# Kernel optimization log

Hardware: AMD Instinct MI355X
Metric: run time of the kernel (lower is better)

The kernel has to match this reference:

```python
import jax, jax.numpy as jnp
import numpy as np

B, C, T, V = 32, 96, 256, 25
BC = C // 4   # TCN branch channels
E = C // 4    # adyn embed dim (max(C//4, 8))


def hswish(x):
    return x * jnp.clip(x + 3.0, 0.0, 6.0) / 6.0


def bn(x, p):
    # p: [4, c] = (gamma, beta, running_mean, running_var); x: [B, c, T, V]
    g, b, rm, rv = p[0], p[1], p[2], p[3]
    inv = jax.lax.rsqrt(rv + 1e-5)
    return (x - rm[:, None, None]) * (g * inv)[:, None, None] + b[:, None, None]


def conv1x1(x, w):
    # w: [O, I]
    return jnp.einsum('bctv,oc->botv', x, w)


def tconv(x, w, stride, dil):
    # temporal conv, kernel 3 on T axis; w: [O, I, 3]
    return jax.lax.conv_general_dilated(
        x, w[:, :, :, None], window_strides=(stride, 1),
        padding=((dil, dil), (0, 0)), rhs_dilation=(dil, 1),
        dimension_numbers=('NCHW', 'OIHW', 'NCHW'))


def _forward(x, A_gcn, W_gcn, gcn_bn, Wp, W_adyn, adyn_gate,
             se_w1, se_b1, se_w2, se_b2,
             pa_w, pa_bn, ta_w, ta_bn, pb_w, pb_bn, tb_w, tb_bn,
             pc_w, pc_bn, pd_w, pd_bn, intra_idx, inter_idx):
    res = x
    # --- BRASP: channel-cyclic shift along joint axis (Shift-GCN style) ---
    sh = (jnp.arange(V)[None, :] + jnp.arange(C)[:, None]) % V  # [C, V]
    x = jnp.take_along_axis(x, sh[None, :, None, :], axis=3)
    # --- SGPShift: half channels gather via intra neighbors, half via inter ---
    h = C // 2
    x = jnp.concatenate([x[:, :h][..., intra_idx], x[:, h:][..., inter_idx]], axis=1)
    # --- multi-partition graph conv: y = mean_k Conv1x1_k(x @ A_k) ---
    xa = jnp.einsum('bctv,kvw->kbctw', x, A_gcn)           # [K,B,C,T,V]
    y = jnp.einsum('kbctw,koc->botw', xa, W_gcn) / A_gcn.shape[0]
    # --- dynamic adjacency (adyn) ---
    emb = jnp.einsum('bcv,ec->bev', x.mean(axis=2), Wp)    # proj then mean over T (linear)
    emb = emb / (jnp.linalg.norm(emb, axis=1, keepdims=True) + 1e-12)
    A_dyn = jnp.einsum('bev,bew->bvw', emb, emb)           # [B,V,V]
    x_dyn = jnp.einsum('bctv,bvw->bctw', x, A_dyn)
    y = y + jax.nn.sigmoid(adyn_gate) * conv1x1(x_dyn, W_adyn)
    x = hswish(bn(y, gcn_bn))
    # --- ChannelSE ---
    s = x.mean(axis=(2, 3))                                 # [B, C]
    z = jax.nn.sigmoid(jnp.dot(jax.nn.relu(jnp.dot(s, se_w1.T) + se_b1), se_w2.T) + se_b2)
    x = x * z[:, :, None, None]
    # --- MultiScaleTCN (stride 1, 4 branches of C//4 channels) ---
    a = hswish(bn(conv1x1(x, pa_w), pa_bn))
    a = bn(tconv(a, ta_w, 1, 1), ta_bn)
    b_ = hswish(bn(conv1x1(x, pb_w), pb_bn))
    b_ = bn(tconv(b_, tb_w, 1, 2), tb_bn)
    c_ = bn(conv1x1(x, pc_w), pc_bn)
    c_ = jax.lax.reduce_window(c_, -jnp.inf, jax.lax.max,
                               (1, 1, 3, 1), (1, 1, 1, 1),
                               [(0, 0), (0, 0), (1, 1), (0, 0)])
    d_ = bn(conv1x1(x, pd_w), pd_bn)
    xt = jnp.concatenate([a, b_, c_, d_], axis=1)           # [B, C, T, V]
    # --- residual + out activation (in==out, stride 1 -> identity residual) ---
    return hswish(xt + res)


def setup_inputs() -> dict:
    key = jax.random.key(0)
    ks = jax.random.split(key, 24)

    def n(k, shape, s=0.1):
        return jax.random.normal(k, shape, jnp.float32) * s

    def mkbn(k, c):
        k1, k2, k3, k4 = jax.random.split(k, 4)
        return jnp.stack([1.0 + 0.1 * jax.random.normal(k1, (c,)),
                          0.1 * jax.random.normal(k2, (c,)),
                          0.1 * jax.random.normal(k3, (c,)),
                          0.5 + jax.random.uniform(k4, (c,))])

    A = jax.random.uniform(ks[1], (3, V, V))
    A = A / (A.sum(-1, keepdims=True) + 1e-6)  # row-normalized structural adjacencies
    return dict(
        x=jax.random.normal(ks[0], (B, C, T, V), jnp.float32),
        intra_idx=jax.random.randint(ks[2], (V,), 0, V),
        inter_idx=jax.random.randint(ks[3], (V,), 0, V),
        A_gcn=A,
        W_gcn=n(ks[4], (3, C, C)),
        gcn_bn=mkbn(ks[5], C),
        Wp=n(ks[6], (E, C)),
        W_adyn=n(ks[7], (C, C)),
        adyn_gate=jnp.float32(-4.0),
        se_w1=n(ks[8], (BC, C)), se_b1=jnp.zeros((BC,), jnp.float32),
        se_w2=n(ks[9], (C, BC)), se_b2=jnp.zeros((C,), jnp.float32),
        pa_w=n(ks[10], (BC, C)), pa_bn=mkbn(ks[11], BC),
        ta_w=n(ks[12], (BC, BC, 3)), ta_bn=mkbn(ks[13], BC),
        pb_w=n(ks[14], (BC, C)), pb_bn=mkbn(ks[15], BC),
        tb_w=n(ks[16], (BC, BC, 3)), tb_bn=mkbn(ks[17], BC),
        pc_w=n(ks[18], (BC, C)), pc_bn=mkbn(ks[19], BC),
        pd_w=n(ks[20], (BC, C)), pd_bn=mkbn(ks[21], BC),
    )


def reference(x, intra_idx, inter_idx, A_gcn, W_gcn, gcn_bn, Wp, W_adyn, adyn_gate,
              se_w1, se_b1, se_w2, se_b2,
              pa_w, pa_bn, ta_w, ta_bn, pb_w, pb_bn, tb_w, tb_bn,
              pc_w, pc_bn, pd_w, pd_bn):
    return _forward(x, A_gcn, W_gcn, gcn_bn, Wp, W_adyn, adyn_gate,
                    se_w1, se_b1, se_w2, se_b2,
                    pa_w, pa_bn, ta_w, ta_bn, pb_w, pb_bn, tb_w, tb_bn,
                    pc_w, pc_bn, pd_w, pd_bn, intra_idx, inter_idx)
```

## Files before the change

### kernel.cpp

```cpp
#include <hip/hip_runtime.h>
#include <math.h>

#define NB 32
#define NC 96
#define NT 256
#define NV 25
#define NBC 24
#define NE 24
#define CV (NC * NV)
#define EV (NE * NV)
#define NK4 384
#define NN 6400
#define ACOLS 112
#define APAD 40

typedef __attribute__((ext_vector_type(8))) short bf16x8;
typedef __attribute__((ext_vector_type(4))) float f32x4;

__device__ __forceinline__ float hswish(float x) {
    return x * fminf(fmaxf(x + 3.f, 0.f), 6.f) * (1.f / 6.f);
}
__device__ __forceinline__ float bnval(float x, const float* p, int n, int c) {
    return (x - p[2 * n + c]) * p[c] * rsqrtf(p[3 * n + c] + 1e-5f) + p[n + c];
}
__device__ __forceinline__ unsigned short f2bf(float f) {
    unsigned u = __float_as_uint(f);
    u += 0x7fffu + ((u >> 16) & 1u);
    return (unsigned short)(u >> 16);
}
__device__ __forceinline__ float bf2f(unsigned short us) {
    return __uint_as_float((unsigned)us << 16);
}

__global__ __launch_bounds__(256) void k_mean(const float* __restrict__ x,
                                              const int* __restrict__ intra,
                                              const int* __restrict__ inter,
                                              float* __restrict__ xm,
                                              unsigned short* __restrict__ xsh) {
    int bc = blockIdx.x;
    int c = bc % NC;
    int tid = threadIdx.x;
    __shared__ int colL[NV];
    if (tid < NV) {
        int s0 = (c < NC / 2) ? intra[tid] : inter[tid];
        colL[tid] = (s0 + c) % NV;
    }
    __syncthreads();
    const float* xp = x + (size_t)bc * NT * NV + (size_t)tid * NV;
    float a[NV];
#pragma unroll
    for (int v = 0; v < NV; ++v) a[v] = xp[v];
    unsigned short row[32];
#pragma unroll
    for (int v = 0; v < NV; ++v) row[v] = f2bf(a[colL[v]]);
#pragma unroll
    for (int v = NV; v < 32; ++v) row[v] = 0;
    bf16x8* dst = (bf16x8*)(xsh + ((size_t)bc * NT + tid) * 32);
#pragma unroll
    for (int s = 0; s < 4; ++s) dst[s] = ((bf16x8*)row)[s];
    __shared__ float part[4][NV];
    int lane = tid & 63, wid = tid >> 6;
#pragma unroll
    for (int v = 0; v < NV; ++v) {
        float val = a[v];
        for (int off = 32; off > 0; off >>= 1) val += __shfl_down(val, off, 64);
        if (lane == 0) part[wid][v] = val;
    }
    __syncthreads();
    if (tid < NV) {
        float s = part[0][tid] + part[1][tid] + part[2][tid] + part[3][tid];
        xm[bc * NV + tid] = s * (1.0f / NT);
    }
}

__global__ __launch_bounds__(256) void k_adyn(const float* __restrict__ xm,
                                              const float* __restrict__ Wp,
                                              const int* __restrict__ intra,
                                              const int* __restrict__ inter,
                                              const float* __restrict__ Agcn,
                                              const float* __restrict__ gate,
                                              unsigned short* __restrict__ acat) {
    int b = blockIdx.x, tid = threadIdx.x;
    __shared__ float xms[CV];
    __shared__ float embs[EV];
    __shared__ float nrm[NV];
    __shared__ float Ads[NV * NV];
    for (int i = tid; i < CV; i += 256) xms[i] = xm[b * CV + i];
    __syncthreads();
    for (int i = tid; i < EV; i += 256) {
        int e = i / NV, v = i % NV;
        int iv = intra[v], ev2 = inter[v];
        float acc = 0.f;
        for (int c = 0; c < NC; ++c) {
            int s0 = (c < NC / 2) ? iv : ev2;
            int col = (s0 + c) % NV;
            acc = fmaf(xms[c * NV + col], Wp[e * NC + c], acc);
        }
        embs[e * NV + v] = acc;
    }
    __syncthreads();
    if (tid < NV) {
        float acc = 0.f;
        for (int e = 0; e < NE; ++e) {
            float t = embs[e * NV + tid];
            acc = fmaf(t, t, acc);
        }
        nrm[tid] = sqrtf(acc) + 1e-12f;
    }
    __syncthreads();
    for (int i = tid; i < NV * NV; i += 256) {
        int v = i / NV, w = i % NV;
        float acc = 0.f;
        for (int e = 0; e < NE; ++e)
            acc = fmaf(embs[e * NV + v], embs[e * NV + w], acc);
        Ads[i] = acc / (nrm[v] * nrm[w]);
    }
    __syncthreads();
    float sg = 1.f / (1.f + expf(-gate[0]));
    for (int i = tid; i < ACOLS * APAD; i += 256) {
        int col = i / APAD, v = i % APAD;
        float val = 0.f;
        if (col < 100 && v < NV) {
            int j = col / NV, w = col % NV;
            if (j < 3) val = Agcn[(j * NV + v) * NV + w] * (1.f / 3.f);
            else val = sg * Ads[v * NV + w];
        }
        acat[(size_t)b * ACOLS * APAD + i] = f2bf(val);
    }
}

__global__ __launch_bounds__(256) void k_wcat(const float* __restrict__ Wg,
                                              const float* __restrict__ Wa,
                                              unsigned short* __restrict__ wcat) {
    int i = blockIdx.x * 256 + threadIdx.x;
    if (i >= NC * NK4) return;
    int o = i / NK4, kc = i % NK4;
    int j = kc / NC, c = kc % NC;
    float v = (j < 3) ? Wg[(j * NC + o) * NC + c] : Wa[o * NC + c];
    wcat[i] = f2bf(v);
}

__global__ __launch_bounds__(256) void k_twp(const float* __restrict__ ta_w,
                                             const float* __restrict__ tb_w,
                                             unsigned short* __restrict__ wtw) {
    int i = blockIdx.x * 256 + threadIdx.x;
    if (i >= 2 * 32 * 96) return;
    int br = i / (32 * 96), rem = i % (32 * 96);
    int o = rem / 96, k = rem % 96;
    float v = 0.f;
    if (o < 24 && k < 72) {
        int i3 = k / 24, c2 = k % 24;
        v = (br ? tb_w : ta_w)[(o * 24 + c2) * 3 + i3];
    }
    wtw[i] = f2bf(v);
}

__global__ __launch_bounds__(256) void k_xa(const unsigned short* __restrict__ xsh,
                                            const unsigned short* __restrict__ acat,
                                            unsigned short* __restrict__ xa, int b0) {
    int blk = blockIdx.x;
    int b = b0 + blk / 384;
    int r0 = (blk % 384) * 64;
    int tid = threadIdx.x;
    __shared__ __align__(16) unsigned short Xs[64][APAD];
    __shared__ __align__(16) unsigned short Bs[ACOLS][APAD];
    {
        const bf16x8* src = (const bf16x8*)(acat + (size_t)b * ACOLS * APAD);
        bf16x8* dst = (bf16x8*)&Bs[0][0];
        for (int i = tid; i < ACOLS * APAD / 8; i += 256) dst[i] = src[i];
    }
    {
        const bf16x8* src = (const bf16x8*)(xsh + ((size_t)b * NC * NT + r0) * 32);
        int row = tid >> 2, s = tid & 3;
        *(bf16x8*)&Xs[row][s * 8] = src[tid];
    }
    __syncthreads();
    int lane = tid & 63, wv = tid >> 6;
    int lr = lane & 15, kg = lane >> 4;
    bf16x8 a = *(const bf16x8*)&Xs[wv * 16 + lr][kg * 8];
    f32x4 acc[7];
#pragma unroll
    for (int nt = 0; nt < 7; ++nt) {
        f32x4 z = {0.f, 0.f, 0.f, 0.f};
        bf16x8 bb = *(const bf16x8*)&Bs[nt * 16 + lr][kg * 8];
        acc[nt] = __builtin_amdgcn_mfma_f32_16x16x32_bf16(a, bb, z, 0, 0, 0);
    }
#pragma unroll
    for (int nt = 0; nt < 7; ++nt) {
        int colbase = nt * 16 + lr;
        if (colbase < 100) {
            int j = colbase / NV, w = colbase % NV;
#pragma unroll
            for (int i = 0; i < 4; ++i) {
                int r = r0 + wv * 16 + kg * 4 + i;
                int c = r >> 8, t = r & 255;
                xa[((size_t)b * NK4 + j * NC + c) * NN + t * NV + w] = f2bf(acc[nt][i]);
            }
        }
    }
}

__global__ __launch_bounds__(256) void k_gemm(const unsigned short* __restrict__ xa,
                                              const unsigned short* __restrict__ wcat,
                                              const float* __restrict__ gbn,
                                              unsigned short* __restrict__ x3, int b0) {
    int blk = blockIdx.x;
    int b = b0 + blk / 100;
    int n0 = (blk % 100) * 64;
    int tid = threadIdx.x;
    __shared__ __align__(16) unsigned short Wpan[NC][APAD];
    __shared__ __align__(16) unsigned short Xp[64 * APAD];
    int lane = tid & 63, wv = tid >> 6;
    int lr = lane & 15, kg = lane >> 4;
    f32x4 acc[6];
#pragma unroll
    for (int mt = 0; mt < 6; ++mt) acc[mt] = (f32x4){0.f, 0.f, 0.f, 0.f};

    int kp = (tid & 127) >> 3;
    int seg = tid & 7;
    int wi = tid - 128;

    for (int kt = 0; kt < 12; ++kt) {
        int k0 = kt * 32;
        __syncthreads();
        if (tid < 128) {
            const unsigned short* src0 = xa + ((size_t)b * NK4 + k0 + 2 * kp) * NN + n0 + seg * 8;
            bf16x8 va = *(const bf16x8*)src0;
            bf16x8 vb = *(const bf16x8*)(src0 + NN);
            char* base = (char*)&Xp[0];
#pragma unroll
            for (int e = 0; e < 8; ++e) {
                int n = seg * 8 + e;
                int g = (kp >> 2) ^ (n & 3) ^ ((n >> 3) & 3);
                unsigned pk = (unsigned)(unsigned short)va[e] |
                              ((unsigned)(unsigned short)vb[e] << 16);
                *(unsigned*)(base + n * 80 + g * 16 + (kp & 3) * 4) = pk;
            }
        } else {
#pragma unroll
            for (int r = 0; r < 3; ++r) {
                int idx = r * 128 + wi;
                int o = idx >> 2, s4 = idx & 3;
                *(bf16x8*)&Wpan[o][s4 * 8] = *(const bf16x8*)(wcat + o * NK4 + k0 + s4 * 8);
            }
        }
        __syncthreads();
        int nl = wv * 16 + lr;
        int g = kg ^ (nl & 3) ^ ((nl >> 3) & 3);
        bf16x8 bb = *(const bf16x8*)((const char*)&Xp[0] + nl * 80 + g * 16);
#pragma unroll
        for (int mt = 0; mt < 6; ++mt) {
            bf16x8 af = *(const bf16x8*)&Wpan[mt * 16 + lr][kg * 8];
            acc[mt] = __builtin_amdgcn_mfma_f32_16x16x32_bf16(af, bb, acc[mt], 0, 0, 0);
        }
    }
    int n = n0 + wv * 16 + lr;
#pragma unroll
    for (int mt = 0; mt < 6; ++mt) {
#pragma unroll
        for (int i = 0; i < 4; ++i) {
            int o = mt * 16 + kg * 4 + i;
            float val = acc[mt][i];
            val = hswish(bnval(val, gbn, NC, o));
            x3[((size_t)b * NC + o) * NN + n] = f2bf(val);
        }
    }
}

__global__ __launch_bounds__(256) void k_sred(const unsigned short* __restrict__ x3,
                                              float* __restrict__ s) {
    int bc = blockIdx.x, tid = threadIdx.x;
    const unsigned short* p = x3 + (size_t)bc * NT * NV;
    float acc = 0.f;
    for (int i = tid; i < NN / 8; i += 256) {
        bf16x8 v = *(const bf16x8*)(p + i * 8);
#pragma unroll
        for (int e = 0; e < 8; ++e) acc += bf2f((unsigned short)v[e]);
    }
    for (int off = 32; off > 0; off >>= 1) acc += __shfl_down(acc, off, 64);
    __shared__ float part[4];
    if ((tid & 63) == 0) part[tid >> 6] = acc;
    __syncthreads();
    if (tid == 0) s[bc] = (part[0] + part[1] + part[2] + part[3]) / (float)(NT * NV);
}

__global__ __launch_bounds__(128) void k_se(const float* __restrict__ s,
                                            const float* __restrict__ w1,
                                            const float* __restrict__ b1,
                                            const float* __restrict__ w2,
                                            const float* __restrict__ b2,
                                            float* __restrict__ z) {
    int b = blockIdx.x, tid = threadIdx.x;
    __shared__ float sl[NC], hl[NBC];
    if (tid < NC) sl[tid] = s[b * NC + tid];
    __syncthreads();
    if (tid < NBC) {
        float acc = b1[tid];
        for (int c = 0; c < NC; ++c) acc = fmaf(w1[tid * NC + c], sl[c], acc);
        hl[tid] = fmaxf(acc, 0.f);
    }
    __syncthreads();
    if (tid < NC) {
        float acc = b2[tid];
        for (int j = 0; j < NBC; ++j) acc = fmaf(w2[tid * NBC + j], hl[j], acc);
        z[b * NC + tid] = 1.f / (1.f + expf(-acc));
    }
}

__global__ __launch_bounds__(256) void k_pww(const float* __restrict__ z,
                                             const float* __restrict__ pa_w,
                                             const float* __restrict__ pb_w,
                                             const float* __restrict__ pc_w,
                                             const float* __restrict__ pd_w,
                                             unsigned short* __restrict__ wse) {
    int i = blockIdx.x * 256 + threadIdx.x;
    if (i >= NB * NC * NC) return;
    int b = i / (NC * NC), rem = i % (NC * NC);
    int o = rem / NC, c = rem % NC;
    int br = o / NBC, lc = o % NBC;
    const float* P = (br == 0) ? pa_w : (br == 1) ? pb_w : (br == 2) ? pc_w : pd_w;
    wse[i] = f2bf(P[lc * NC + c] * z[b * NC + c]);
}

__global__ __launch_bounds__(256) void k_pwg(const unsigned short* __restrict__ x3,
                                             const unsigned short* __restrict__ wse,
                                             const float* __restrict__ pa_bn,
                                             const float* __restrict__ pb_bn,
                                             const float* __restrict__ pc_bn,
                                             const float* __restrict__ pd_bn,
                                             unsigned short* __restrict__ ut48,
                                             unsigned short* __restrict__ u2) {
    int blk = blockIdx.x;
    int b = blk / 50;
    int n0 = (blk % 50) * 128;
    int tid = threadIdx.x;
    __shared__ __align__(16) char SMEM[33280];
    unsigned short* Wpan = (unsigned short*)SMEM;
    unsigned short* Xp = Wpan + 3 * NC * APAD;
    float* Yt = (float*)SMEM;

    int lane = tid & 63, wv = tid >> 6;
    int lr = lane & 15, kg = lane >> 4;
    f32x4 acc[6][2];
#pragma unroll
    for (int mt = 0; mt < 6; ++mt)
#pragma unroll
        for (int nn = 0; nn < 2; ++nn) acc[mt][nn] = (f32x4){0.f, 0.f, 0.f, 0.f};

    const unsigned short* wb = wse + (size_t)b * NC * NC;
    for (int i = tid; i < 3 * NC * 4; i += 256) {
        int kt = i / (NC * 4), rem = i % (NC * 4);
        int o = rem >> 2, s4 = rem & 3;
        *(bf16x8*)&Wpan[(kt * NC + o) * APAD + s4 * 8] =
            *(const bf16x8*)(wb + o * NC + kt * 32 + s4 * 8);
    }

    int kp = tid >> 4;
    int seg = tid & 15;
    const unsigned short* x3b = x3 + (size_t)b * NC * NN;

    for (int kt = 0; kt < 3; ++kt) {
        int k0 = kt * 32;
        {
            const unsigned short* src0 = x3b + (size_t)(k0 + 2 * kp) * NN + n0 + seg * 8;
            bf16x8 va = *(const bf16x8*)src0;
            bf16x8 vb = *(const bf16x8*)(src0 + NN);
            char* base = (char*)Xp;
#pragma unroll
            for (int e = 0; e < 8; ++e) {
                int n = seg * 8 + e;
                int g = (kp >> 2) ^ (n & 3) ^ ((n >> 3) & 3);
                unsigned pk = (unsigned)(unsigned short)va[e] |
                              ((unsigned)(unsigned short)vb[e] << 16);
                *(unsigned*)(base + n * 80 + g * 16 + (kp & 3) * 4) = pk;
            }
        }
        __syncthreads();
        bf16x8 afr[6];
#pragma unroll
        for (int mt = 0; mt < 6; ++mt)
            afr[mt] = *(const bf16x8*)&Wpan[(kt * NC + mt * 16 + lr) * APAD + kg * 8];
#pragma unroll
        for (int nn = 0; nn < 2; ++nn) {
            int nl = (wv * 2 + nn) * 16 + lr;
            int g = kg ^ (nl & 3) ^ ((nl >> 3) & 3);
            bf16x8 bb = *(const bf16x8*)((const char*)Xp + nl * 80 + g * 16);
#pragma unroll
            for (int mt = 0; mt < 6; ++mt)
                acc[mt][nn] = __builtin_amdgcn_mfma_f32_16x16x32_bf16(afr[mt], bb, acc[mt][nn], 0, 0, 0);
        }
        __syncthreads();
    }
#pragma unroll
    for (int mt = 0; mt < 6; ++mt)
#pragma unroll
        for (int nn = 0; nn < 2; ++nn) {
            int nl = (wv * 2 + nn) * 16 + lr;
#pragma unroll
            for (int i = 0; i < 4; ++i) {
                int o = mt * 16 + kg * 4 + i;
                int br = o / NBC, lc = o % NBC;
                const float* bnp = (br == 0) ? pa_bn : (br == 1) ? pb_bn
                                 : (br == 2) ? pc_bn : pd_bn;
                float val = bnval(acc[mt][nn][i], bnp, NBC, lc);
                if (br < 2) {
                    Yt[nl * 49 + o] = hswish(val);
                } else {
                    u2[((size_t)b * 48 + (o - 48)) * NN + n0 + nl] = f2bf(val);
                }
            }
        }
    __syncthreads();
    for (int i = tid; i < 128 * 6; i += 256) {
        int n = i / 6, og = i % 6;
        bf16x8 v;
#pragma unroll
        for (int e = 0; e < 8; ++e) v[e] = (short)f2bf(Yt[n * 49 + og * 8 + e]);
        *(bf16x8*)(ut48 + ((size_t)b * NN + n0 + n) * 48 + og * 8) = v;
    }
}

__global__ __launch_bounds__(256) void k_tcnm(const unsigned short* __restrict__ ut48,
                                              const unsigned short* __restrict__ wtw,
                                              const float* __restrict__ ta_bn,
                                              const float* __restrict__ tb_bn,
                                              unsigned short* __restrict__ uc) {
    int blk = blockIdx.x;
    int b = blk / 50, n0 = (blk % 50) * 128;
    int tid = threadIdx.x;
    __shared__ __align__(16) unsigned short Ut[240][56];
    int wn = n0 - 56;
    const unsigned short* utb = ut48 + (size_t)b * NN * 48;
    for (int idx = tid; idx < 240 * 6; idx += 256) {
        int row = idx / 6, seg = idx % 6;
        int n = wn + row;
        bf16x8 val = {0, 0, 0, 0, 0, 0, 0, 0};
        if (n >= 0 && n < NN)
            val = *(const bf16x8*)(utb + (size_t)n * 48 + seg * 8);
        *(bf16x8*)&Ut[row][seg * 8] = val;
    }
    int lane = tid & 63, wave = tid >> 6;
    int lr = lane & 15, kg = lane >> 4;
    int br = wave >> 1, mh = wave & 1;
    int dn = 25 + br * 25;
    bf16x8 af[3];
#pragma unroll
    for (int kt = 0; kt < 3; ++kt)
        af[kt] = *(const bf16x8*)(wtw + (br * 32 + mh * 16 + lr) * 96 + kt * 32 + kg * 8);
    __syncthreads();

    f32x4 acc[8];
#pragma unroll
    for (int nt = 0; nt < 8; ++nt) acc[nt] = (f32x4){0.f, 0.f, 0.f, 0.f};
#pragma unroll
    for (int kt = 0; kt < 3; ++kt) {
        int g = kt * 4 + kg;
        int gg = (g > 8) ? 8 : g;
        int i3 = gg / 3;
        int c2b = (gg - i3 * 3) * 8;
        int roff = 56 + (i3 - 1) * dn;
        int colb = br * 24 + c2b;
#pragma unroll
        for (int nt = 0; nt < 8; ++nt) {
            int nrow = nt * 16 + lr + roff;
            bf16x8 bb = *(const bf16x8*)&Ut[nrow][colb];
            acc[nt] = __builtin_amdgcn_mfma_f32_16x16x32_bf16(af[kt], bb, acc[nt], 0, 0, 0);
        }
    }
    const float* bnp = br ? tb_bn : ta_bn;
    int ml = mh * 16 + kg * 4;
#pragma unroll
    for (int ii = 0; ii < 4; ++ii) {
        int ol = ml + ii;
        if (ol < 24) {
            int oc = br * 24 + ol;
#pragma unroll
            for (int nt = 0; nt < 8; ++nt) {
                int n = n0 + nt * 16 + lr;
                uc[((size_t)b * 48 + oc) * NN + n] = f2bf(bnval(acc[nt][ii], bnp, NBC, ol));
            }
        }
    }
}

__global__ __launch_bounds__(256) void k_fin(const unsigned short* __restrict__ uc,
                                             const unsigned short* __restrict__ u2,
                                             const float* __restrict__ x,
                                             float* __restrict__ out) {
    const int JV = NN / 8;
    const int NVEC = NB * NC * JV;
    for (int vid = blockIdx.x * 256 + threadIdx.x; vid < NVEC; vid += gridDim.x * 256) {
        int j = vid % JV;
        int bc = vid / JV;
        int ch = bc % NC, b = bc / NC;
        int n = j * 8;
        float val[8];
        if (ch < 48) {
            bf16x8 t = *(const bf16x8*)(uc + ((size_t)b * 48 + ch) * NN + n);
#pragma unroll
            for (int e = 0; e < 8; ++e) val[e] = bf2f((unsigned short)t[e]);
        } else if (ch < 72) {
            const unsigned short* p = u2 + ((size_t)b * 48 + (ch - 48)) * NN;
            if (j >= 4 && j <= JV - 5) {
                bf16x8 M = *(const bf16x8*)(p + n);
                bf16x8 Lm = *(const bf16x8*)(p + n - 24);
                bf16x8 Rp = *(const bf16x8*)(p + n + 24);
                float lm1 = bf2f(p[n - 25]);
                float rp1 = bf2f(p[n + 32]);
#pragma unroll
                for (int e = 0; e < 8; ++e) {
                    float vm = (e == 0) ? lm1 : bf2f((unsigned short)Lm[e - 1]);
                    float vp = (e == 7) ? rp1 : bf2f((unsigned short)Rp[e + 1]);
                    val[e] = fmaxf(fmaxf(bf2f((unsigned short)M[e]), vm), vp);
                }
            } else {
#pragma unroll
                for (int e = 0; e < 8; ++e) {
                    int ne = n + e;
                    float m = bf2f(p[ne]);
                    if (ne >= 25) m = fmaxf(m, bf2f(p[ne - 25]));
                    if (ne + 25 < NN) m = fmaxf(m, bf2f(p[ne + 25]));
                    val[e] = m;
                }
            }
        } else {
            bf16x8 t = *(const bf16x8*)(u2 + ((size_t)b * 48 + (ch - 48)) * NN + n);
#pragma unroll
            for (int e = 0; e < 8; ++e) val[e] = bf2f((unsigned short)t[e]);
        }
        const float* xp = x + (size_t)bc * NN + n;
        float* op = out + (size_t)bc * NN + n;
        f32x4 x0 = *(const f32x4*)xp;
        f32x4 x1 = *(const f32x4*)(xp + 4);
        f32x4 o0, o1;
#pragma unroll
        for (int e = 0; e < 4; ++e) o0[e] = hswish(val[e] + x0[e]);
#pragma unroll
        for (int e = 0; e < 4; ++e) o1[e] = hswish(val[e + 4] + x1[e]);
        *(f32x4*)op = o0;
        *(f32x4*)(op + 4) = o1;
    }
}

extern "C" void kernel_launch(void* const* d_in, const int* in_sizes, int n_in,
                              void* d_out, int out_size, void* d_ws, size_t ws_size,
                              hipStream_t stream) {
    const float* x = (const float*)d_in[0];
    const int* intra = (const int*)d_in[1];
    const int* inter = (const int*)d_in[2];
    const float* A_gcn = (const float*)d_in[3];
    const float* W_gcn = (const float*)d_in[4];
    const float* gcn_bn = (const float*)d_in[5];
    const float* Wp = (const float*)d_in[6];
    const float* W_adyn = (const float*)d_in[7];
    const float* gate = (const float*)d_in[8];
    const float* se_w1 = (const float*)d_in[9];
    const float* se_b1 = (const float*)d_in[10];
    const float* se_w2 = (const float*)d_in[11];
    const float* se_b2 = (const float*)d_in[12];
    const float* pa_w = (const float*)d_in[13];
    const float* pa_bn = (const float*)d_in[14];
    const float* ta_w = (const float*)d_in[15];
    const float* ta_bn = (const float*)d_in[16];
    const float* pb_w = (const float*)d_in[17];
    const float* pb_bn = (const float*)d_in[18];
    const float* tb_w = (const float*)d_in[19];
    const float* tb_bn = (const float*)d_in[20];
    const float* pc_w = (const float*)d_in[21];
    const float* pc_bn = (const float*)d_in[22];
    const float* pd_w = (const float*)d_in[23];
    const float* pd_bn = (const float*)d_in[24];
    float* out = (float*)d_out;

    char* wsb = (char*)d_ws;
    const size_t ELEMS = (size_t)NB * NC * NT * NV;
    const size_t HALF = (size_t)NB * NN * 48;
    const size_t XSH = (size_t)NB * NC * NT * 32;
    unsigned short* x3 = (unsigned short*)wsb;
    unsigned short* ut48 = x3 + ELEMS;
    unsigned short* u2 = ut48 + HALF;
    unsigned short* uc = u2 + HALF;
    unsigned short* xsh = uc + HALF;
    float* xm = (float*)(xsh + XSH);
    float* sb = xm + NB * NC * NV;
    float* zb = sb + NB * NC;
    unsigned short* wcat = (unsigned short*)(zb + NB * NC);
    unsigned short* acat = wcat + NC * NK4;
    unsigned short* wse = acat + NB * ACOLS * APAD;
    unsigned short* wtw = wse + (size_t)NB * NC * NC;
    unsigned short* xabuf = wtw + 2 * 32 * 96;
    size_t base_bytes = (char*)xabuf - wsb;

    int chunk = 1;
    const int cands[6] = {32, 16, 8, 4, 2, 1};
    for (int ci = 0; ci < 6; ++ci) {
        size_t need = base_bytes + (size_t)cands[ci] * NK4 * NN * 2;
        if (need <= ws_size) { chunk = cands[ci]; break; }
    }

    k_mean<<<NB * NC, 256, 0, stream>>>(x, intra, inter, xm, xsh);
    k_adyn<<<NB, 256, 0, stream>>>(xm, Wp, intra, inter, A_gcn, gate, acat);
    k_wcat<<<(NC * NK4 + 255) / 256, 256, 0, stream>>>(W_gcn, W_adyn, wcat);
    k_twp<<<(2 * 32 * 96 + 255) / 256, 256, 0, stream>>>(ta_w, tb_w, wtw);
    for (int b0 = 0; b0 < NB; b0 += chunk) {
        k_xa<<<chunk * 384, 256, 0, stream>>>(xsh, acat, xabuf, b0);
        k_gemm<<<chunk * 100, 256, 0, stream>>>(xabuf, wcat, gcn_bn, x3, b0);
    }
    k_sred<<<NB * NC, 256, 0, stream>>>(x3, sb);
    k_se<<<NB, 128, 0, stream>>>(sb, se_w1, se_b1, se_w2, se_b2, zb);
    k_pww<<<(NB * NC * NC + 255) / 256, 256, 0, stream>>>(zb, pa_w, pb_w, pc_w, pd_w, wse);
    k_pwg<<<NB * 50, 256, 0, stream>>>(x3, wse, pa_bn, pb_bn, pc_bn, pd_bn, ut48, u2);
    k_tcnm<<<NB * 50, 256, 0, stream>>>(ut48, wtw, ta_bn, tb_bn, uc);
    k_fin<<<2048, 256, 0, stream>>>(uc, u2, x, out);
}
```

Baseline: 267.5 us.

## Stage xa output through LDS for coalesced stores and prefetch GEMM tiles

Measured after the change: 250.9 us. 1.07x faster.

```diff
diff --git a/kernel.cpp b/kernel.cpp
--- a/kernel.cpp
+++ b/kernel.cpp
@@ -160,10 +160,13 @@
                                             unsigned short* __restrict__ xa, int b0) {
     int blk = blockIdx.x;
     int b = b0 + blk / 384;
-    int r0 = (blk % 384) * 64;
+    int rblk = blk % 384;
+    int r0 = rblk * 64;
     int tid = threadIdx.x;
-    __shared__ __align__(16) unsigned short Xs[64][APAD];
-    __shared__ __align__(16) unsigned short Bs[ACOLS][APAD];
+    __shared__ __align__(16) unsigned short SM[7040];
+    unsigned short (*Xs)[APAD] = (unsigned short(*)[APAD])SM;
+    unsigned short (*Bs)[APAD] = (unsigned short(*)[APAD])(SM + 64 * APAD);
+    unsigned short* Yx = SM;
     {
         const bf16x8* src = (const bf16x8*)(acat + (size_t)b * ACOLS * APAD);
         bf16x8* dst = (bf16x8*)&Bs[0][0];
@@ -185,17 +188,28 @@
         bf16x8 bb = *(const bf16x8*)&Bs[nt * 16 + lr][kg * 8];
         acc[nt] = __builtin_amdgcn_mfma_f32_16x16x32_bf16(a, bb, z, 0, 0, 0);
     }
+    __syncthreads();
+    int tl = wv * 16 + kg * 4;
 #pragma unroll
     for (int nt = 0; nt < 7; ++nt) {
         int colbase = nt * 16 + lr;
         if (colbase < 100) {
-            int j = colbase / NV, w = colbase % NV;
-#pragma unroll
-            for (int i = 0; i < 4; ++i) {
-                int r = r0 + wv * 16 + kg * 4 + i;
-                int c = r >> 8, t = r & 255;
-                xa[((size_t)b * NK4 + j * NC + c) * NN + t * NV + w] = f2bf(acc[nt][i]);
-            }
+            int j = colbase / NV, w = colbase - NV * j;
+#pragma unroll
+            for (int i = 0; i < 4; ++i)
+                Yx[j * 1600 + (tl + i) * NV + w] = f2bf(acc[nt][i]);
+        }
+    }
+    __syncthreads();
+    int c = rblk >> 2, tbase = (rblk & 3) * 64;
+    unsigned short* outb = xa + ((size_t)b * NK4 + c) * NN + tbase * NV;
+#pragma unroll
+    for (int it = 0; it < 4; ++it) {
+        int idx = it * 256 + tid;
+        if (idx < 800) {
+            int j = idx / 200, off = idx % 200;
+            *(bf16x8*)(outb + (size_t)j * NC * NN + off * 8) =
+                *(const bf16x8*)&Yx[j * 1600 + off * 8];
         }
     }
 }
@@ -209,7 +223,7 @@
     int n0 = (blk % 100) * 64;
     int tid = threadIdx.x;
     __shared__ __align__(16) unsigned short Wpan[NC][APAD];
-    __shared__ __align__(16) unsigned short Xp[64 * APAD];
+    __shared__ __align__(16) unsigned short Xp[64 * 20 * 2];
     int lane = tid & 63, wv = tid >> 6;
     int lr = lane & 15, kg = lane >> 4;
     f32x4 acc[6];
@@ -219,35 +233,65 @@
     int kp = (tid & 127) >> 3;
     int seg = tid & 7;
     int wi = tid - 128;
+    const unsigned short* srcx = xa + ((size_t)b * NK4 + 2 * kp) * NN + n0 + seg * 8;
+
+    bf16x8 va, vb, w0r, w1r, w2r;
+    if (tid < 128) {
+        va = *(const bf16x8*)srcx;
+        vb = *(const bf16x8*)(srcx + NN);
+    } else {
+#pragma unroll
+        for (int r = 0; r < 3; ++r) {
+            int idx = r * 128 + wi;
+            int o = idx >> 2, s4 = idx & 3;
+            bf16x8 t = *(const bf16x8*)(wcat + o * NK4 + s4 * 8);
+            if (r == 0) w0r = t; else if (r == 1) w1r = t; else w2r = t;
+        }
+    }
 
     for (int kt = 0; kt < 12; ++kt) {
-        int k0 = kt * 32;
         __syncthreads();
         if (tid < 128) {
-            const unsigned short* src0 = xa + ((size_t)b * NK4 + k0 + 2 * kp) * NN + n0 + seg * 8;
-            bf16x8 va = *(const bf16x8*)src0;
-            bf16x8 vb = *(const bf16x8*)(src0 + NN);
             char* base = (char*)&Xp[0];
 #pragma unroll
             for (int e = 0; e < 8; ++e) {
                 int n = seg * 8 + e;
-                int g = (kp >> 2) ^ (n & 3) ^ ((n >> 3) & 3);
+                int q = (n & 56) | ((n + seg) & 7);
+                int g = (kp >> 2) ^ (e & 3) ^ (seg & 3);
                 unsigned pk = (unsigned)(unsigned short)va[e] |
                               ((unsigned)(unsigned short)vb[e] << 16);
-                *(unsigned*)(base + n * 80 + g * 16 + (kp & 3) * 4) = pk;
+                *(unsigned*)(base + q * 80 + g * 16 + (kp & 3) * 4) = pk;
             }
         } else {
 #pragma unroll
             for (int r = 0; r < 3; ++r) {
                 int idx = r * 128 + wi;
                 int o = idx >> 2, s4 = idx & 3;
-                *(bf16x8*)&Wpan[o][s4 * 8] = *(const bf16x8*)(wcat + o * NK4 + k0 + s4 * 8);
+                bf16x8 t = (r == 0) ? w0r : (r == 1) ? w1r : w2r;
+                *(bf16x8*)&Wpan[o][s4 * 8] = t;
             }
         }
         __syncthreads();
+        if (kt < 11) {
+            int k0n = (kt + 1) * 32;
+            if (tid < 128) {
+                const unsigned short* sx = srcx + (size_t)k0n * NN;
+                va = *(const bf16x8*)sx;
+                vb = *(const bf16x8*)(sx + NN);
+            } else {
+#pragma unroll
+                for (int r = 0; r < 3; ++r) {
+                    int idx = r * 128 + wi;
+                    int o = idx >> 2, s4 = idx & 3;
+                    bf16x8 t = *(const bf16x8*)(wcat + o * NK4 + k0n + s4 * 8);
+                    if (r == 0) w0r = t; else if (r == 1) w1r = t; else w2r = t;
+                }
+            }
+        }
         int nl = wv * 16 + lr;
+        int q = (nl & 56) | ((nl + (nl >> 3)) & 7);
         int g = kg ^ (nl & 3) ^ ((nl >> 3) & 3);
-        bf16x8 bb = *(const bf16x8*)((const char*)&Xp[0] + nl * 80 + g * 16);
+        bf16x8 bb = *(const bf16x8*)((const char*)&Xp[0] + q * 80 + g * 16);
 #pragma unroll
         for (int mt = 0; mt < 6; ++mt) {
             bf16x8 af = *(const bf16x8*)&Wpan[mt * 16 + lr][kg * 8];
```

## Store xa in k-interleaved blocked layout and double-buffer weight panel in gemm

Applied to the files above, without the earlier changes.

Result: faster. 249.7 us (-6.7%).

```diff
diff --git a/kernel.cpp b/kernel.cpp
--- a/kernel.cpp
+++ b/kernel.cpp
@@ -157,22 +157,26 @@
 
 __global__ __launch_bounds__(256) void k_xa(const unsigned short* __restrict__ xsh,
                                             const unsigned short* __restrict__ acat,
-                                            unsigned short* __restrict__ xa, int b0) {
+                                            unsigned short* __restrict__ xaf, int b0) {
     int blk = blockIdx.x;
     int b = b0 + blk / 384;
-    int r0 = (blk % 384) * 64;
+    int rblk = blk % 384;
+    int cg = rblk >> 5, tg = rblk & 31;
     int tid = threadIdx.x;
-    __shared__ __align__(16) unsigned short Xs[64][APAD];
-    __shared__ __align__(16) unsigned short Bs[ACOLS][APAD];
+    __shared__ __align__(16) unsigned short SM[7040];
+    unsigned short (*Xs)[APAD] = (unsigned short(*)[APAD])SM;
+    unsigned short (*Bs)[APAD] = (unsigned short(*)[APAD])(SM + 64 * APAD);
+    unsigned short* Yx = SM;
     {
         const bf16x8* src = (const bf16x8*)(acat + (size_t)b * ACOLS * APAD);
         bf16x8* dst = (bf16x8*)&Bs[0][0];
         for (int i = tid; i < ACOLS * APAD / 8; i += 256) dst[i] = src[i];
     }
     {
-        const bf16x8* src = (const bf16x8*)(xsh + ((size_t)b * NC * NT + r0) * 32);
         int row = tid >> 2, s = tid & 3;
-        *(bf16x8*)&Xs[row][s * 8] = src[tid];
+        const unsigned short* src = xsh +
+            (((size_t)(b * NC + cg * 8 + (row >> 3))) * NT + tg * 8 + (row & 7)) * 32 + s * 8;
+        *(bf16x8*)&Xs[row][s * 8] = *(const bf16x8*)src;
     }
     __syncthreads();
     int lane = tid & 63, wv = tid >> 6;
@@ -185,22 +189,35 @@
         bf16x8 bb = *(const bf16x8*)&Bs[nt * 16 + lr][kg * 8];
         acc[nt] = __builtin_amdgcn_mfma_f32_16x16x32_bf16(a, bb, z, 0, 0, 0);
     }
+    __syncthreads();
 #pragma unroll
     for (int nt = 0; nt < 7; ++nt) {
         int colbase = nt * 16 + lr;
         if (colbase < 100) {
-            int j = colbase / NV, w = colbase % NV;
+            int j = colbase / NV, w = colbase - NV * j;
 #pragma unroll
             for (int i = 0; i < 4; ++i) {
-                int r = r0 + wv * 16 + kg * 4 + i;
-                int c = r >> 8, t = r & 255;
-                xa[((size_t)b * NK4 + j * NC + c) * NN + t * NV + w] = f2bf(acc[nt][i]);
-            }
-        }
-    }
-}
-
-__global__ __launch_bounds__(256) void k_gemm(const unsigned short* __restrict__ xa,
+                int row = wv * 16 + kg * 4 + i;
+                int cl = row >> 3, tl = row & 7;
+                Yx[(j * 200 + tl * NV + w) * 8 + cl] = f2bf(acc[nt][i]);
+            }
+        }
+    }
+    __syncthreads();
+    unsigned short* xb = xaf + (size_t)b * NK4 * NN;
+#pragma unroll
+    for (int it = 0; it < 4; ++it) {
+        int idx = it * 256 + tid;
+        if (idx < 800) {
+            int j = idx / 200, tw = idx % 200;
+            int kgi = 12 * j + cg;
+            *(bf16x8*)(xb + ((size_t)kgi * NN + tg * 200 + tw) * 8) =
+                *(const bf16x8*)&Yx[(j * 200 + tw) * 8];
+        }
+    }
+}
+
+__global__ __launch_bounds__(256) void k_gemm(const unsigned short* __restrict__ xaf,
                                               const unsigned short* __restrict__ wcat,
                                               const float* __restrict__ gbn,
                                               unsigned short* __restrict__ x3, int b0) {
@@ -208,50 +225,59 @@
     int b = b0 + blk / 100;
     int n0 = (blk % 100) * 64;
     int tid = threadIdx.x;
-    __shared__ __align__(16) unsigned short Wpan[NC][APAD];
-    __shared__ __align__(16) unsigned short Xp[64 * APAD];
+    __shared__ __align__(16) unsigned short Wpan[2][NC][APAD];
     int lane = tid & 63, wv = tid >> 6;
     int lr = lane & 15, kg = lane >> 4;
     f32x4 acc[6];
 #pragma unroll
     for (int mt = 0; mt < 6; ++mt) acc[mt] = (f32x4){0.f, 0.f, 0.f, 0.f};
 
-    int kp = (tid & 127) >> 3;
-    int seg = tid & 7;
-    int wi = tid - 128;
-
+    const unsigned short* bsrc = xaf + (size_t)b * NK4 * NN
+                               + ((size_t)kg * NN + n0 + wv * 16 + lr) * 8;
+    bf16x8 bnext = *(const bf16x8*)bsrc;
+    {
+        for (int i2 = tid; i2 < 384; i2 += 256) {
+            int o = i2 >> 2, s4 = i2 & 3;
+            *(bf16x8*)&Wpan[0][o][s4 * 8] = *(const bf16x8*)(wcat + o * NK4 + s4 * 8);
+        }
+    }
     for (int kt = 0; kt < 12; ++kt) {
-        int k0 = kt * 32;
         __syncthreads();
-        if (tid < 128) {
-            const unsigned short* src0 = xa + ((size_t)b * NK4 + k0 + 2 * kp) * NN + n0 + seg * 8;
-            bf16x8 va = *(const bf16x8*)src0;
-            bf16x8 vb = *(const bf16x8*)(src0 + NN);
-            char* base = (char*)&Xp[0];
-#pragma unroll
-            for (int e = 0; e < 8; ++e) {
-                int n = seg * 8 + e;
-                int g = (kp >> 2) ^ (n & 3) ^ ((n >> 3) & 3);
-                unsigned pk = (unsigned)(unsigned short)va[e] |
-                              ((unsigned)(unsigned short)vb[e] << 16);
-                *(unsigned*)(base + n * 80 + g * 16 + (kp & 3) * 4) = pk;
-            }
-        } else {
-#pragma unroll
-            for (int r = 0; r < 3; ++r) {
-                int idx = r * 128 + wi;
-                int o = idx >> 2, s4 = idx & 3;
-                *(bf16x8*)&Wpan[o][s4 * 8] = *(const bf16x8*)(wcat + o * NK4 + k0 + s4 * 8);
-            }
-        }
-        __syncthreads();
-        int nl = wv * 16 + lr;
-        int g = kg ^ (nl & 3) ^ ((nl >> 3) & 3);
-        bf16x8 bb = *(const bf16x8*)((const char*)&Xp[0] + nl * 80 + g * 16);
-#pragma unroll
-        for (int mt = 0; mt < 6; ++mt) {
-            bf16x8 af = *(const bf16x8*)&Wpan[mt * 16 + lr][kg * 8];
-            acc[mt] = __builtin_amdgcn_mfma_f32_16x16x32_bf16(af, bb, acc[mt], 0, 0, 0);
+        int cb = kt & 1;
+        bf16x8 bcur = bnext;
+        bf16x8 af[6];
+#pragma unroll
+        for (int mt = 0; mt < 6; ++mt)
+            af[mt] = *(const bf16x8*)&Wpan[cb][mt * 16 + lr][kg * 8];
+        bf16x8 w0, w1;
+        bool more = (kt < 11);
+        if (more) {
+            bnext = *(const bf16x8*)(bsrc + (size_t)(kt + 1) * 4 * NN * 8);
+            int k0n = (kt + 1) * 32;
+            {
+                int o = tid >> 2, s4 = tid & 3;
+                w0 = *(const bf16x8*)(wcat + o * NK4 + k0n + s4 * 8);
+            }
+            if (tid < 128) {
+                int i2 = 256 + tid;
+                int o = i2 >> 2, s4 = i2 & 3;
+                w1 = *(const bf16x8*)(wcat + o * NK4 + k0n + s4 * 8);
+            }
+        }
+#pragma unroll
+        for (int mt = 0; mt < 6; ++mt)
+            acc[mt] = __builtin_amdgcn_mfma_f32_16x16x32_bf16(af[mt], bcur, acc[mt], 0, 0, 0);
+        if (more) {
+            int nb = (kt + 1) & 1;
+            {
+                int o = tid >> 2, s4 = tid & 3;
+                *(bf16x8*)&Wpan[nb][o][s4 * 8] = w0;
+            }
+            if (tid < 128) {
+                int i2 = 256 + tid;
+                int o = i2 >> 2, s4 = i2 & 3;
+                *(bf16x8*)&Wpan[nb][o][s4 * 8] = w1;
+            }
         }
     }
     int n = n0 + wv * 16 + lr;
```
